# Kernel tuning notes

Measured on AMD Instinct MI355X. Metric: run time of the kernel, lower is better.

## Reference

```python
import jax, jax.numpy as jnp
import numpy as np

B, T, S1, S2 = 8, 64, 128, 128
TD, SD, V, PAD = 512, 512, 32000, 0
EXT = V + S1 + S2
EPS = 1e-5


def _ln(x):
    # F.layer_norm with no affine params (biased variance, eps=1e-5)
    m = x.mean(axis=-1, keepdims=True)
    v = ((x - m) ** 2).mean(axis=-1, keepdims=True)
    return (x - m) / jnp.sqrt(v + EPS)


def _cross_attention(q, k, q_mask, k_mask, attn_w, attn_b, v_vec):
    # attn(cat(q,k)) == q @ Wq^T + k @ Wk^T + b, computed without materializing the concat
    Wq = attn_w[:, :TD]          # [TD, TD] (query part of weight: cat order is (query, key))
    Wk = attn_w[:, TD:]          # [TD, SD]
    sq = jnp.einsum('btd,ed->bte', q, Wq)   # [B,T,TD]
    sk = jnp.einsum('bsd,ed->bse', k, Wk)   # [B,S,TD]
    energy = jnp.tanh(sq[:, :, None, :] + sk[:, None, :, :] + attn_b)  # [B,T,S,TD]
    scores = jnp.einsum('btse,e->bts', energy, v_vec)                  # [B,T,S]
    out_att = scores * k_mask[:, None, :] * q_mask[:, :, None]
    masked = jnp.where((k_mask == PAD)[:, None, :], -jnp.inf, scores)
    attn = jax.nn.softmax(masked, axis=-1)
    weight = jnp.einsum('bts,bsd->btd', attn, k) * q_mask[:, :, None]  # [B,T,SD]
    return out_att, weight


def _scatter_copy(att, map_idx):
    # index_put_(accumulate=True) into [B,T,EXT]
    copy = jnp.zeros((B, T, EXT), dtype=att.dtype)
    b_idx = jnp.arange(B)[:, None, None]
    t_idx = jnp.arange(T)[None, :, None]
    m_idx = map_idx[:, None, :]
    return copy.at[b_idx, t_idx, m_idx].add(att)


def setup_inputs() -> dict:
    key = jax.random.key(0)
    ks = jax.random.split(key, 14)
    sc = 0.02
    return {
        'tgt_dec_out': jax.random.normal(ks[0], (B, T, TD), jnp.float32),
        'src1_key': jax.random.normal(ks[1], (B, S1, SD), jnp.float32),
        'src2_key': jax.random.normal(ks[2], (B, S2, SD), jnp.float32),
        'src1_map_idx': jax.random.randint(ks[3], (B, S1), 0, EXT),
        'src2_map_idx': jax.random.randint(ks[4], (B, S2), 0, EXT),
        'out_fc_w': jax.random.normal(ks[5], (V, TD), jnp.float32) * sc,
        'out_fc_b': jnp.zeros((V,), jnp.float32),
        'attn1_w': jax.random.normal(ks[6], (TD, SD + TD), jnp.float32) * sc,
        'attn1_b': jnp.zeros((TD,), jnp.float32),
        'v1': jax.random.normal(ks[7], (TD,), jnp.float32) * sc,
        'attn2_w': jax.random.normal(ks[8], (TD, SD + TD), jnp.float32) * sc,
        'attn2_b': jnp.zeros((TD,), jnp.float32),
        'v2': jax.random.normal(ks[9], (TD,), jnp.float32) * sc,
        'gate_w': jax.random.normal(ks[10], (3, 2 * SD + TD), jnp.float32) * sc,
        'gate_b': jnp.zeros((3,), jnp.float32),
    }


def reference(tgt_dec_out, src1_key, src2_key, src1_map_idx, src2_map_idx,
              out_fc_w, out_fc_b, attn1_w, attn1_b, v1, attn2_w, attn2_b, v2,
              gate_w, gate_b):
    tgt_output = _ln(jnp.einsum('btd,vd->btv', tgt_dec_out, out_fc_w) + out_fc_b)
    tgt_output = jnp.pad(tgt_output, ((0, 0), (0, 0), (0, S1 + S2)), constant_values=float(PAD))

    tgt_mask = jnp.sign(jnp.abs(tgt_dec_out).sum(-1))   # [B,T]
    src1_mask = jnp.sign(jnp.abs(src1_key).sum(-1))     # [B,S1]
    src2_mask = jnp.sign(jnp.abs(src2_key).sum(-1))     # [B,S2]

    att1, c1 = _cross_attention(tgt_dec_out, src1_key, tgt_mask, src1_mask, attn1_w, attn1_b, v1)
    att1 = _ln(att1)
    copy_output1 = _scatter_copy(att1, src1_map_idx)

    att2, c2 = _cross_attention(tgt_dec_out, src2_key, tgt_mask, src2_mask, attn2_w, attn2_b, v2)
    att2 = _ln(att2)
    copy_output2 = _scatter_copy(att2, src2_map_idx)

    gate_in = jnp.concatenate([tgt_dec_out, c1, c2], axis=-1)  # [B,T,TD+2*SD]
    p = jax.nn.softmax(jnp.einsum('btd,pd->btp', gate_in, gate_w) + gate_b, axis=-1)  # [B,T,3]

    output = (tgt_output * p[..., 0:1]
              + copy_output1 * p[..., 1:2]
              + copy_output2 * p[..., 2:3])
    return output
```

## Files before the change

kernel.cpp:

```cpp
#include <hip/hip_runtime.h>

#define NB 8
#define NT 64
#define NS 128
#define TDIM 512
#define NV 32000
#define NEXT 32256
#define NBT 512
#define LNEPS 1e-5f
#define CLG 2.8853900817779268f

typedef unsigned short u16;
typedef __attribute__((ext_vector_type(8))) short short8;
typedef __attribute__((ext_vector_type(4))) short s16x4;
typedef __attribute__((ext_vector_type(4))) float f32x4;

__device__ __forceinline__ float bf2f(u16 u){ union{unsigned int i; float f;} v; v.i = ((unsigned int)u)<<16; return v.f; }
__device__ __forceinline__ u16 f2bf(float f){ union{float f; unsigned int i;} v; v.f=f; unsigned int r = v.i + 0x7FFFu + ((v.i>>16)&1u); return (u16)(r>>16); }
__device__ __forceinline__ float wsum(float v){
  v += __shfl_xor(v,32); v += __shfl_xor(v,16); v += __shfl_xor(v,8);
  v += __shfl_xor(v,4);  v += __shfl_xor(v,2);  v += __shfl_xor(v,1); return v; }
__device__ __forceinline__ float wmax(float v){
  v = fmaxf(v,__shfl_xor(v,32)); v = fmaxf(v,__shfl_xor(v,16)); v = fmaxf(v,__shfl_xor(v,8));
  v = fmaxf(v,__shfl_xor(v,4));  v = fmaxf(v,__shfl_xor(v,2));  v = fmaxf(v,__shfl_xor(v,1)); return v; }

#define GL2LDS(gp, lp) __builtin_amdgcn_global_load_lds( \
    (__attribute__((address_space(1))) void*)(void*)(gp), \
    (__attribute__((address_space(3))) void*)(void*)(lp), 16, 0, 0)

__global__ __launch_bounds__(256) void k_cast(const float* tgt, const float* s1, const float* s2,
    const float* a1w, const float* a2w,
    u16* tgtb, u16* s1b, u16* s2b, u16* a1wb, u16* a2wb, float* msk)
{
  int blk = blockIdx.x;
  const float* src; u16* dst; int base;
  if(blk < 128){       src=tgt; dst=tgtb;  base=blk; }
  else if(blk < 384){  src=s1;  dst=s1b;   base=blk-128; }
  else if(blk < 640){  src=s2;  dst=s2b;   base=blk-384; }
  else if(blk < 896){  src=a1w; dst=a1wb;  base=blk-640; }
  else {               src=a2w; dst=a2wb;  base=blk-896; }
  size_t off = (size_t)base*2048 + (size_t)threadIdx.x*8;
  float4 x0 = *(const float4*)(src+off);
  float4 x1 = *(const float4*)(src+off+4);
  float xs[8] = {x0.x,x0.y,x0.z,x0.w,x1.x,x1.y,x1.z,x1.w};
  short8 r;
  #pragma unroll
  for(int j=0;j<8;++j) r[j] = (short)f2bf(xs[j]);
  *(short8*)(dst+off) = r;
  if(blk < 640){
    float a = 0.f;
    #pragma unroll
    for(int j=0;j<8;++j) a += fabsf(xs[j]);
    a = wsum(a);
    if((threadIdx.x&63)==0){
      int w = threadIdx.x>>6;
      int midx;
      if(blk<128)      midx = blk*4 + w;
      else if(blk<384) midx = 512 + (blk-128)*4 + w;
      else             midx = 1536 + (blk-384)*4 + w;
      msk[midx] = (a>0.f) ? 1.f : 0.f;
    }
  }
}

template<int MODE>
__device__ __forceinline__ void gemm_core(const u16* A, int lda, const u16* W, int ldw,
    float* Cf, int ldc, const float* bias, int K, int bm, int bn, float scale)
{
  __shared__ u16 Al[128*32];
  __shared__ u16 Wl[128*32];
  const int tid = threadIdx.x, lane = tid&63, wv = tid>>6;
  const int wm = wv>>1, wn = wv&1;
  const int fr = lane&15, fq = lane>>4;
  const int lrow = lane>>2;
  const int lcol = (lane&3)*8;
  f32x4 acc[4][4] = {};
  for(int k0=0;k0<K;k0+=32){
    #pragma unroll
    for(int r=0;r<2;++r){
      int c = wv + 4*r;
      int row = c*16 + lrow;
      const u16* ga = A + (size_t)(bm+row)*lda + k0 + lcol;
      const u16* gw = W + (size_t)(bn+row)*ldw + k0 + lcol;
      GL2LDS(ga, &Al[c*512]);
      GL2LDS(gw, &Wl[c*512]);
    }
    __syncthreads();
    short8 af[4], bfr[4];
    #pragma unroll
    for(int m=0;m<4;++m) af[m] = *(const short8*)&Al[(wm*64 + m*16 + fr)*32 + fq*8];
    #pragma unroll
    for(int n=0;n<4;++n) bfr[n] = *(const short8*)&Wl[(wn*64 + n*16 + fr)*32 + fq*8];
    #pragma unroll
    for(int m=0;m<4;++m)
      #pragma unroll
      for(int n=0;n<4;++n)
        acc[m][n] = __builtin_amdgcn_mfma_f32_16x16x32_bf16(af[m], bfr[n], acc[m][n], 0,0,0);
    __syncthreads();
  }
  #pragma unroll
  for(int m=0;m<4;++m)
    #pragma unroll
    for(int n=0;n<4;++n)
      #pragma unroll
      for(int i=0;i<4;++i){
        int row = bm + wm*64 + m*16 + fq*4 + i;
        int col = bn + wn*64 + n*16 + fr;
        float bv = bias ? bias[col] : 0.f;
        Cf[(size_t)row*ldc + col] = (acc[m][n][i] + bv)*scale;
      }
}

__global__ __launch_bounds__(256) void k_proj(const u16* tgt, const u16* s1, const u16* s2,
    const u16* w1, const u16* w2, const float* b1, const float* b2,
    float* sq1, float* sk1, float* sq2, float* sk2)
{
  int z = blockIdx.z;
  int Mt = (z&1) ? 1024 : 512;
  int bm = blockIdx.y*128; if(bm >= Mt) return;
  const u16* A = (z&1) ? ((z>>1) ? s2 : s1) : tgt;
  const u16* W = ((z>>1) ? w2 : w1) + ((z&1) ? TDIM : 0);
  float* Cf = (z==0) ? sq1 : (z==1) ? sk1 : (z==2) ? sq2 : sk2;
  const float* bias = (z&1) ? nullptr : ((z>>1) ? b2 : b1);
  gemm_core<2>(A, TDIM, W, 2*TDIM, Cf, TDIM, bias, TDIM, bm, blockIdx.x*128, CLG);
}

__global__ __launch_bounds__(256) void k_big(const u16* A, const float* Wf, const float* bias,
                                             u16* logits, float2* pstats)
{
  int lid = (blockIdx.x&7)*125 + (blockIdx.x>>3);
  int bm = (lid&3)*128, bn = (lid>>2)*128;
  __shared__ u16 Al[128*32];
  __shared__ u16 Wl[128*32];
  __shared__ float ps_s[2][128], pq_s[2][128];
  const int tid = threadIdx.x, lane = tid&63, wv = tid>>6;
  const int wm = wv>>1, wn = wv&1;
  const int fr = lane&15, fq = lane>>4;
  const int lrow = lane>>2;
  const int lcol = (lane&3)*8;
  f32x4 acc[4][4] = {};
  for(int k0=0;k0<512;k0+=32){
    #pragma unroll
    for(int r=0;r<2;++r){
      int c = wv + 4*r;
      int row = c*16 + lrow;
      GL2LDS(A + (size_t)(bm+row)*512 + k0 + lcol, &Al[c*512]);
    }
    #pragma unroll
    for(int j=0;j<4;++j){
      int idx = j*256 + tid;
      int row = idx>>3, c = idx&7;
      float4 w4 = *(const float4*)(Wf + (size_t)(bn+row)*512 + k0 + c*4);
      s16x4 o;
      o[0]=(short)f2bf(w4.x); o[1]=(short)f2bf(w4.y); o[2]=(short)f2bf(w4.z); o[3]=(short)f2bf(w4.w);
      *(s16x4*)&Wl[row*32 + c*4] = o;
    }
    __syncthreads();
    short8 af[4], bfr[4];
    #pragma unroll
    for(int m=0;m<4;++m) af[m] = *(const short8*)&Al[(wm*64 + m*16 + fr)*32 + fq*8];
    #pragma unroll
    for(int n=0;n<4;++n) bfr[n] = *(const short8*)&Wl[(wn*64 + n*16 + fr)*32 + fq*8];
    #pragma unroll
    for(int m=0;m<4;++m)
      #pragma unroll
      for(int n=0;n<4;++n)
        acc[m][n] = __builtin_amdgcn_mfma_f32_16x16x32_bf16(af[m], bfr[n], acc[m][n], 0,0,0);
    __syncthreads();
  }
  #pragma unroll
  for(int m=0;m<4;++m){
    float rs_[4]={0,0,0,0}, rq_[4]={0,0,0,0};
    #pragma unroll
    for(int n=0;n<4;++n)
      #pragma unroll
      for(int i=0;i<4;++i){
        int row = bm + wm*64 + m*16 + fq*4 + i;
        int col = bn + wn*64 + n*16 + fr;
        float v = acc[m][n][i] + bias[col];
        logits[(size_t)row*NV + col] = f2bf(v);
        rs_[i] += v; rq_[i] += v*v;
      }
    #pragma unroll
    for(int i=0;i<4;++i){
      float a=rs_[i], q=rq_[i];
      a+=__shfl_xor(a,1); a+=__shfl_xor(a,2); a+=__shfl_xor(a,4); a+=__shfl_xor(a,8);
      q+=__shfl_xor(q,1); q+=__shfl_xor(q,2); q+=__shfl_xor(q,4); q+=__shfl_xor(q,8);
      if(fr==0){ int lr = wm*64 + m*16 + fq*4 + i; ps_s[wn][lr]=a; pq_s[wn][lr]=q; }
    }
  }
  __syncthreads();
  if(tid<128){
    float2 pv;
    pv.x = ps_s[0][tid]+ps_s[1][tid];
    pv.y = pq_s[0][tid]+pq_s[1][tid];
    pstats[(size_t)(bm+tid)*250 + (lid>>2)] = pv;
  }
}

__global__ __launch_bounds__(256) void k_energy(
  const float* sq1, const float* sq2, const float* sk1, const float* sk2,
  const float* v1p, const float* v2p, float* pene)
{
  int lid = (blockIdx.x&7)*128 + (blockIdx.x>>3);
  int src = lid>>9, b = (lid>>6)&7, tc = (lid>>4)&3, sc = (lid>>2)&3, eq = lid&3;
  int tid = threadIdx.x;
  const float* SQ = src? sq2:sq1;
  const float* SK = src? sk2:sk1;
  const float* vp = src? v2p:v1p;
  int t0 = tc*16, s0 = sc*32;
  int strow = tid&31, trow = tid>>5;

  __shared__ float sk_lds[32*65];
  float acc_a = 0.f, acc_b = 0.f;
  const float* sqa = SQ + (size_t)(b*64 + t0 + trow)*512;
  const float* sqb = sqa + 8*512;

  for(int ec=eq*2; ec<eq*2+2; ++ec){
    {
      int r = tid>>3, c0 = (tid&7)*8;
      const float* sp = SK + (size_t)(b*128 + s0 + r)*512 + ec*64 + c0;
      float4 A0 = *(const float4*)sp;
      float4 A1 = *(const float4*)(sp+4);
      float* dp = &sk_lds[r*65 + c0];
      dp[0]=A0.x; dp[1]=A0.y; dp[2]=A0.z; dp[3]=A0.w;
      dp[4]=A1.x; dp[5]=A1.y; dp[6]=A1.z; dp[7]=A1.w;
    }
    __syncthreads();
    #pragma unroll
    for(int sub=0; sub<4; ++sub){
      int e0 = ec*64 + sub*16;
      float4 V0 = *(const float4*)(vp+e0),    V1 = *(const float4*)(vp+e0+4);
      float4 V2 = *(const float4*)(vp+e0+8),  V3 = *(const float4*)(vp+e0+12);
      float4 QA0 = *(const float4*)(sqa+e0),  QA1 = *(const float4*)(sqa+e0+4);
      float4 QA2 = *(const float4*)(sqa+e0+8),QA3 = *(const float4*)(sqa+e0+12);
      float4 QB0 = *(const float4*)(sqb+e0),  QB1 = *(const float4*)(sqb+e0+4);
      float4 QB2 = *(const float4*)(sqb+e0+8),QB3 = *(const float4*)(sqb+e0+12);
      float vv[16] = {V0.x,V0.y,V0.z,V0.w,V1.x,V1.y,V1.z,V1.w,V2.x,V2.y,V2.z,V2.w,V3.x,V3.y,V3.z,V3.w};
      float qa[16] = {QA0.x,QA0.y,QA0.z,QA0.w,QA1.x,QA1.y,QA1.z,QA1.w,QA2.x,QA2.y,QA2.z,QA2.w,QA3.x,QA3.y,QA3.z,QA3.w};
      float qb[16] = {QB0.x,QB0.y,QB0.z,QB0.w,QB1.x,QB1.y,QB1.z,QB1.w,QB2.x,QB2.y,QB2.z,QB2.w,QB3.x,QB3.y,QB3.z,QB3.w};
      const float* skr = &sk_lds[strow*65 + sub*16];
      #pragma unroll
      for(int e=0;e<16;++e){
        float skv = skr[e];
        float ya = qa[e] + skv;
        float yb = qb[e] + skv;
        float ra = __builtin_amdgcn_rcpf(__builtin_amdgcn_exp2f(ya) + 1.f);
        float rb = __builtin_amdgcn_rcpf(__builtin_amdgcn_exp2f(yb) + 1.f);
        acc_a = __builtin_fmaf(vv[e], ra, acc_a);
        acc_b = __builtin_fmaf(vv[e], rb, acc_b);
      }
    }
    __syncthreads();
  }
  size_t ia = (size_t)((eq*2+src)*512 + b*64 + t0 + trow)*128 + s0 + strow;
  pene[ia] = acc_a;
  pene[ia + 8*128] = acc_b;
}

__global__ __launch_bounds__(256) void k_sm(
  const float* pene, const float* v1p, const float* v2p,
  const float* k1g, const float* k2g, const float* msk,
  float* al1, float* al2, float* c1, float* c2)
{
  int lid = (blockIdx.x&7)*32 + (blockIdx.x>>3);
  int src = lid>>7, b = (lid>>4)&7, tq = lid&15;
  int tid = threadIdx.x, lane = tid&63, wv = tid>>6;
  int t = tq*4 + wv, bt = b*64 + t;
  const float* vp = src? v2p:v1p;
  const float* kg = src? k2g:k1g;
  float* al = src? al2:al1;
  float* cc = src? c2:c1;
  const float* km_g = msk + 512 + src*1024 + b*128;
  __shared__ float aw_lds[4][132];
  __shared__ float qm_lds[4];

  {
    float vsp = 0.f;
    #pragma unroll
    for(int r2=0;r2<8;++r2) vsp += vp[lane + 64*r2];
    float Vsum = wsum(vsp);
    float qm = msk[bt];
    float km0 = km_g[lane], km1 = km_g[lane+64];
    size_t pbase = (size_t)(src*512 + bt)*128;
    float p0a = pene[pbase + lane]          + pene[pbase + 131072 + lane];
    float p0b = pene[pbase + 262144 + lane] + pene[pbase + 393216 + lane];
    float p1a = pene[pbase + lane + 64]          + pene[pbase + 131072 + lane + 64];
    float p1b = pene[pbase + 262144 + lane + 64] + pene[pbase + 393216 + lane + 64];
    float s0v = Vsum - 2.f*(p0a + p0b);
    float s1v = Vsum - 2.f*(p1a + p1b);
    float a0 = s0v*km0*qm, a1 = s1v*km1*qm;
    float sm = wsum(a0+a1), sqq = wsum(a0*a0+a1*a1);
    float m0 = km0!=0.f ? s0v : -1e30f;
    float m1 = km1!=0.f ? s1v : -1e30f;
    float mx = wmax(fmaxf(m0,m1));
    float e0 = km0!=0.f ? __expf(s0v-mx) : 0.f;
    float e1 = km1!=0.f ? __expf(s1v-mx) : 0.f;
    float den = wsum(e0+e1);
    float mean = sm/128.f;
    float inv  = rsqrtf(sqq/128.f - mean*mean + LNEPS);
    al[(size_t)bt*128 + lane]      = (a0-mean)*inv;
    al[(size_t)bt*128 + lane + 64] = (a1-mean)*inv;
    float rden = 1.f/den;
    aw_lds[wv][lane]      = e0*rden;
    aw_lds[wv][lane+64]   = e1*rden;
    if(lane==0) qm_lds[wv] = qm;
  }
  __syncthreads();
  {
    float acc[4][2] = {};
    const float* kb = kg + (size_t)b*128*512;
    for(int s=0;s<128;++s){
      float kv0 = kb[(size_t)s*512 + tid];
      float kv1 = kb[(size_t)s*512 + tid + 256];
      #pragma unroll
      for(int w=0;w<4;++w){
        float a = aw_lds[w][s];
        acc[w][0] = __builtin_fmaf(a, kv0, acc[w][0]);
        acc[w][1] = __builtin_fmaf(a, kv1, acc[w][1]);
      }
    }
    #pragma unroll
    for(int w=0;w<4;++w){
      float qm = qm_lds[w];
      size_t o = (size_t)(b*64 + tq*4 + w)*512;
      cc[o + tid]       = qm*acc[w][0];
      cc[o + tid + 256] = qm*acc[w][1];
    }
  }
}

__global__ __launch_bounds__(256) void k_out(const u16* logits, const float2* pstats,
    const float* al1, const float* al2, const float* c1, const float* c2,
    const float* tgt, const float* gw, const float* gb,
    const int* map1, const int* map2, float* out)
{
  int row = blockIdx.x>>2, q = blockIdx.x&3, b = row>>6;
  int tid = threadIdx.x, lane = tid&63, wv = tid>>6;
  __shared__ float gred[4][3], rs[4], rq[4], st[2], pl_s[3];
  __shared__ int hkey[1024];
  __shared__ float hval[1024];
  __shared__ unsigned int bmap[252];

  #pragma unroll
  for(int r=0;r<4;++r){ hkey[tid+256*r] = -1; hval[tid+256*r] = 0.f; }
  if(tid < 252) bmap[tid] = 0u;

  {
    float t0v = tgt[(size_t)row*512+tid], t1v = tgt[(size_t)row*512+tid+256];
    float c10 = c1[(size_t)row*512+tid],  c11 = c1[(size_t)row*512+tid+256];
    float c20 = c2[(size_t)row*512+tid],  c21 = c2[(size_t)row*512+tid+256];
    #pragma unroll
    for(int p=0;p<3;++p){
      const float* gp = gw + p*1536;
      float a = gp[tid]*t0v + gp[tid+256]*t1v
              + gp[512+tid]*c10 + gp[768+tid]*c11
              + gp[1024+tid]*c20 + gp[1280+tid]*c21;
      a = wsum(a);
      if(lane==0) gred[wv][p] = a;
    }
  }
  {
    float s=0.f, qv=0.f;
    if(tid < 250){ float2 pv = pstats[(size_t)row*250 + tid]; s = pv.x; qv = pv.y; }
    s = wsum(s); qv = wsum(qv);
    if(lane==0){ rs[wv]=s; rq[wv]=qv; }
  }
  __syncthreads();
  if(tid==0){
    float S = rs[0]+rs[1]+rs[2]+rs[3];
    float Q = rq[0]+rq[1]+rq[2]+rq[3];
    float mean = S/(float)NV;
    float var  = Q/(float)NV - mean*mean;
    st[0] = mean; st[1] = rsqrtf(var+LNEPS);
    float g0 = gred[0][0]+gred[1][0]+gred[2][0]+gred[3][0] + gb[0];
    float g1 = gred[0][1]+gred[1][1]+gred[2][1]+gred[3][1] + gb[1];
    float g2 = gred[0][2]+gred[1][2]+gred[2][2]+gred[3][2] + gb[2];
    float m = fmaxf(g0, fmaxf(g1, g2));
    float e0=__expf(g0-m), e1=__expf(g1-m), e2=__expf(g2-m);
    float sI = 1.f/(e0+e1+e2);
    pl_s[0]=e0*sI; pl_s[1]=e1*sI; pl_s[2]=e2*sI;
  }
  __syncthreads();

  int elo = q*8064;
  {
    int src = tid>>7, sl = tid&127;
    int e = (src ? map2 : map1)[b*128 + sl];
    if(e >= elo && e < elo+8064){
      float val = pl_s[1+src] * (src ? al2 : al1)[(size_t)row*128 + sl];
      unsigned int h = ((unsigned int)e * 2654435761u) >> 22;
      for(;;){
        int old = atomicCAS(&hkey[h], -1, e);
        if(old == -1 || old == e){ atomicAdd(&hval[h], val); break; }
        h = (h+1) & 1023;
      }
      int rel = e - elo;
      atomicOr(&bmap[rel>>5], 1u << (rel&31));
    }
  }
  __syncthreads();

  float mean = st[0], inv = st[1], p0 = pl_s[0];
  const u16* Lr = logits + (size_t)row*NV;
  float* orow = out + (size_t)row*NEXT;
  for(int i=q*2016+tid; i<(q+1)*2016; i+=256){
    int e0 = i*4;
    float4 r;
    if(e0 < NV){
      const u16* L = &Lr[e0];
      r.x = p0*(bf2f(L[0])-mean)*inv;
      r.y = p0*(bf2f(L[1])-mean)*inv;
      r.z = p0*(bf2f(L[2])-mean)*inv;
      r.w = p0*(bf2f(L[3])-mean)*inv;
    } else { r.x=r.y=r.z=r.w=0.f; }
    int rel = e0 - elo;
    unsigned int w4 = (bmap[rel>>5] >> (rel&31)) & 0xFu;
    if(w4){
      #pragma unroll
      for(int j=0;j<4;++j){
        if(w4 & (1u<<j)){
          int e = e0 + j;
          unsigned int h = ((unsigned int)e * 2654435761u) >> 22;
          while(hkey[h] != e) h = (h+1) & 1023;
          float pv = hval[h];
          if(j==0) r.x += pv; else if(j==1) r.y += pv; else if(j==2) r.z += pv; else r.w += pv;
        }
      }
    }
    *(float4*)&orow[e0] = r;
  }
}

extern "C" void kernel_launch(void* const* d_in, const int* in_sizes, int n_in,
                              void* d_out, int out_size, void* d_ws, size_t ws_size,
                              hipStream_t stream)
{
  const float* tgt  = (const float*)d_in[0];
  const float* s1k  = (const float*)d_in[1];
  const float* s2k  = (const float*)d_in[2];
  const int*   map1 = (const int*)d_in[3];
  const int*   map2 = (const int*)d_in[4];
  const float* ofw  = (const float*)d_in[5];
  const float* ofb  = (const float*)d_in[6];
  const float* a1w  = (const float*)d_in[7];
  const float* a1b  = (const float*)d_in[8];
  const float* v1   = (const float*)d_in[9];
  const float* a2w  = (const float*)d_in[10];
  const float* a2b  = (const float*)d_in[11];
  const float* v2   = (const float*)d_in[12];
  const float* gw   = (const float*)d_in[13];
  const float* gb   = (const float*)d_in[14];

  float* wsf   = (float*)d_ws;
  float* sq1   = wsf;
  float* sq2   = wsf + 262144;
  float* sk1   = wsf + 524288;
  float* sk2   = wsf + 1048576;
  float* al1   = wsf + 1572864;
  float* al2   = wsf + 1638400;
  float* msk   = wsf + 1705984;
  float* c1    = wsf + 1709568;
  float* c2    = wsf + 1971712;
  float* pene  = wsf + 2233856;
  float2* pstats = (float2*)(wsf + 2758144);
  u16*  logits = (u16*)(wsf + 3014144);
  u16*  tgtb   = (u16*)(wsf + 11206144);
  u16*  s1b    = (u16*)(wsf + 11337216);
  u16*  s2b    = (u16*)(wsf + 11599360);
  u16*  a1wb   = (u16*)(wsf + 11861504);
  u16*  a2wb   = (u16*)(wsf + 12123648);
  float* out   = (float*)d_out;

  k_cast   <<<1152, 256, 0, stream>>>(tgt, s1k, s2k, a1w, a2w, tgtb, s1b, s2b, a1wb, a2wb, msk);
  k_proj   <<<dim3(4,8,4), 256, 0, stream>>>(tgtb, s1b, s2b, a1wb, a2wb, a1b, a2b, sq1, sk1, sq2, sk2);
  k_energy <<<1024, 256, 0, stream>>>(sq1, sq2, sk1, sk2, v1, v2, pene);
  k_sm     <<<256, 256, 0, stream>>>(pene, v1, v2, s1k, s2k, msk, al1, al2, c1, c2);
  k_big    <<<1000, 256, 0, stream>>>(tgtb, ofw, ofb, logits, pstats);
  k_out    <<<2048, 256, 0, stream>>>(logits, pstats, al1, al2, c1, c2, tgt, gw, gb, map1, map2, out);
}
```

Measured before the change: 122.4 us.

## Pre-cast output weight to bf16, merge projection and logits GEMMs, stage logits stores

The fp32 output weight is now cast to bf16 in the cast kernel instead of inside the logits GEMM's inner loop, so that GEMM can load both operands with direct global-to-LDS loads. The projection GEMM and the large logits GEMM become one launch, with extra blocks handling the projections. Logits are staged through LDS and written as 16-byte row-contiguous stores instead of scattered 2-byte stores. The cost is an extra pass that reads the 64MB fp32 weight and writes a 32MB bf16 copy every call, plus more LDS and more syncs per block.

```diff
diff --git a/kernel.cpp b/kernel.cpp
--- a/kernel.cpp
+++ b/kernel.cpp
@@ -12,7 +12,6 @@
 
 typedef unsigned short u16;
 typedef __attribute__((ext_vector_type(8))) short short8;
-typedef __attribute__((ext_vector_type(4))) short s16x4;
 typedef __attribute__((ext_vector_type(4))) float f32x4;
 
 __device__ __forceinline__ float bf2f(u16 u){ union{unsigned int i; float f;} v; v.i = ((unsigned int)u)<<16; return v.f; }
@@ -29,8 +28,8 @@
     (__attribute__((address_space(3))) void*)(void*)(lp), 16, 0, 0)
 
 __global__ __launch_bounds__(256) void k_cast(const float* tgt, const float* s1, const float* s2,
-    const float* a1w, const float* a2w,
-    u16* tgtb, u16* s1b, u16* s2b, u16* a1wb, u16* a2wb, float* msk)
+    const float* a1w, const float* a2w, const float* ofw,
+    u16* tgtb, u16* s1b, u16* s2b, u16* a1wb, u16* a2wb, u16* ofwb, float* msk)
 {
   int blk = blockIdx.x;
   const float* src; u16* dst; int base;
@@ -38,7 +37,8 @@
   else if(blk < 384){  src=s1;  dst=s1b;   base=blk-128; }
   else if(blk < 640){  src=s2;  dst=s2b;   base=blk-384; }
   else if(blk < 896){  src=a1w; dst=a1wb;  base=blk-640; }
-  else {               src=a2w; dst=a2wb;  base=blk-896; }
+  else if(blk < 1152){ src=a2w; dst=a2wb;  base=blk-896; }
+  else {               src=ofw; dst=ofwb;  base=blk-1152; }
   size_t off = (size_t)base*2048 + (size_t)threadIdx.x*8;
   float4 x0 = *(const float4*)(src+off);
   float4 x1 = *(const float4*)(src+off+4);
@@ -63,12 +63,9 @@
   }
 }
 
-template<int MODE>
-__device__ __forceinline__ void gemm_core(const u16* A, int lda, const u16* W, int ldw,
+__device__ __forceinline__ void gemm_core2(u16* Al, u16* Wl, const u16* A, int lda, const u16* W, int ldw,
     float* Cf, int ldc, const float* bias, int K, int bm, int bn, float scale)
 {
-  __shared__ u16 Al[128*32];
-  __shared__ u16 Wl[128*32];
   const int tid = threadIdx.x, lane = tid&63, wv = tid>>6;
   const int wm = wv>>1, wn = wv&1;
   const int fr = lane&15, fq = lane>>4;
@@ -111,28 +108,32 @@
       }
 }
 
-__global__ __launch_bounds__(256) void k_proj(const u16* tgt, const u16* s1, const u16* s2,
-    const u16* w1, const u16* w2, const float* b1, const float* b2,
+__global__ __launch_bounds__(256) void k_bigproj(const u16* A, const u16* W, const float* bias,
+    u16* logits, float2* pstats,
+    const u16* s1, const u16* s2, const u16* w1, const u16* w2,
+    const float* b1, const float* b2,
     float* sq1, float* sk1, float* sq2, float* sk2)
 {
-  int z = blockIdx.z;
-  int Mt = (z&1) ? 1024 : 512;
-  int bm = blockIdx.y*128; if(bm >= Mt) return;
-  const u16* A = (z&1) ? ((z>>1) ? s2 : s1) : tgt;
-  const u16* W = ((z>>1) ? w2 : w1) + ((z&1) ? TDIM : 0);
-  float* Cf = (z==0) ? sq1 : (z==1) ? sk1 : (z==2) ? sq2 : sk2;
-  const float* bias = (z&1) ? nullptr : ((z>>1) ? b2 : b1);
-  gemm_core<2>(A, TDIM, W, 2*TDIM, Cf, TDIM, bias, TDIM, bm, blockIdx.x*128, CLG);
-}
-
-__global__ __launch_bounds__(256) void k_big(const u16* A, const float* Wf, const float* bias,
-                                             u16* logits, float2* pstats)
-{
-  int lid = (blockIdx.x&7)*125 + (blockIdx.x>>3);
-  int bm = (lid&3)*128, bn = (lid>>2)*128;
   __shared__ u16 Al[128*32];
   __shared__ u16 Wl[128*32];
   __shared__ float ps_s[2][128], pq_s[2][128];
+  __shared__ u16 c16[2][16][136];
+
+  if(blockIdx.x >= 1000){
+    int p = blockIdx.x - 1000;
+    int z = p>>5, y = (p>>2)&7, x = p&3;
+    int Mt = (z&1) ? 1024 : 512;
+    int bm = y*128; if(bm >= Mt) return;
+    const u16* Ap = (z&1) ? ((z>>1) ? s2 : s1) : A;
+    const u16* Wp = ((z>>1) ? w2 : w1) + ((z&1) ? TDIM : 0);
+    float* Cf = (z==0) ? sq1 : (z==1) ? sk1 : (z==2) ? sq2 : sk2;
+    const float* bp = (z&1) ? nullptr : ((z>>1) ? b2 : b1);
+    gemm_core2(Al, Wl, Ap, TDIM, Wp, 2*TDIM, Cf, TDIM, bp, TDIM, bm, x*128, CLG);
+    return;
+  }
+
+  int lid = (blockIdx.x&7)*125 + (blockIdx.x>>3);
+  int bm = (lid&3)*128, bn = (lid>>2)*128;
   const int tid = threadIdx.x, lane = tid&63, wv = tid>>6;
   const int wm = wv>>1, wn = wv&1;
   const int fr = lane&15, fq = lane>>4;
@@ -145,15 +146,7 @@
       int c = wv + 4*r;
       int row = c*16 + lrow;
       GL2LDS(A + (size_t)(bm+row)*512 + k0 + lcol, &Al[c*512]);
-    }
-    #pragma unroll
-    for(int j=0;j<4;++j){
-      int idx = j*256 + tid;
-      int row = idx>>3, c = idx&7;
-      float4 w4 = *(const float4*)(Wf + (size_t)(bn+row)*512 + k0 + c*4);
-      s16x4 o;
-      o[0]=(short)f2bf(w4.x); o[1]=(short)f2bf(w4.y); o[2]=(short)f2bf(w4.z); o[3]=(short)f2bf(w4.w);
-      *(s16x4*)&Wl[row*32 + c*4] = o;
+      GL2LDS(W + (size_t)(bn+row)*512 + k0 + lcol, &Wl[c*512]);
     }
     __syncthreads();
     short8 af[4], bfr[4];
@@ -168,6 +161,7 @@
         acc[m][n] = __builtin_amdgcn_mfma_f32_16x16x32_bf16(af[m], bfr[n], acc[m][n], 0,0,0);
     __syncthreads();
   }
+
   #pragma unroll
   for(int m=0;m<4;++m){
     float rs_[4]={0,0,0,0}, rq_[4]={0,0,0,0};
@@ -175,10 +169,9 @@
     for(int n=0;n<4;++n)
       #pragma unroll
       for(int i=0;i<4;++i){
-        int row = bm + wm*64 + m*16 + fq*4 + i;
         int col = bn + wn*64 + n*16 + fr;
         float v = acc[m][n][i] + bias[col];
-        logits[(size_t)row*NV + col] = f2bf(v);
+        c16[wm][fq*4+i][wn*64 + n*16 + fr] = f2bf(v);
         rs_[i] += v; rq_[i] += v*v;
       }
     #pragma unroll
@@ -188,8 +181,17 @@
       q+=__shfl_xor(q,1); q+=__shfl_xor(q,2); q+=__shfl_xor(q,4); q+=__shfl_xor(q,8);
       if(fr==0){ int lr = wm*64 + m*16 + fq*4 + i; ps_s[wn][lr]=a; pq_s[wn][lr]=q; }
     }
-  }
-  __syncthreads();
+    __syncthreads();
+    {
+      int band = tid>>7, r = (tid>>3)&15, c0 = (tid&7)*16;
+      int grow = bm + band*64 + m*16 + r;
+      short8 o0 = *(const short8*)&c16[band][r][c0];
+      short8 o1 = *(const short8*)&c16[band][r][c0+8];
+      *(short8*)&logits[(size_t)grow*NV + bn + c0]     = o0;
+      *(short8*)&logits[(size_t)grow*NV + bn + c0 + 8] = o1;
+    }
+    __syncthreads();
+  }
   if(tid<128){
     float2 pv;
     pv.x = ps_s[0][tid]+ps_s[1][tid];
@@ -470,12 +472,13 @@
   u16*  s2b    = (u16*)(wsf + 11599360);
   u16*  a1wb   = (u16*)(wsf + 11861504);
   u16*  a2wb   = (u16*)(wsf + 12123648);
+  u16*  ofwb   = (u16*)(wsf + 12385792);
   float* out   = (float*)d_out;
 
-  k_cast   <<<1152, 256, 0, stream>>>(tgt, s1k, s2k, a1w, a2w, tgtb, s1b, s2b, a1wb, a2wb, msk);
-  k_proj   <<<dim3(4,8,4), 256, 0, stream>>>(tgtb, s1b, s2b, a1wb, a2wb, a1b, a2b, sq1, sk1, sq2, sk2);
+  k_cast   <<<9152, 256, 0, stream>>>(tgt, s1k, s2k, a1w, a2w, ofw, tgtb, s1b, s2b, a1wb, a2wb, ofwb, msk);
+  k_bigproj<<<1128, 256, 0, stream>>>(tgtb, ofwb, ofb, logits, pstats,
+                                      s1b, s2b, a1wb, a2wb, a1b, a2b, sq1, sk1, sq2, sk2);
   k_energy <<<1024, 256, 0, stream>>>(sq1, sq2, sk1, sk2, v1, v2, pene);
   k_sm     <<<256, 256, 0, stream>>>(pene, v1, v2, s1k, s2k, msk, al1, al2, c1, c2);
-  k_big    <<<1000, 256, 0, stream>>>(tgtb, ofw, ofb, logits, pstats);
   k_out    <<<2048, 256, 0, stream>>>(logits, pstats, al1, al2, c1, c2, tgt, gw, gb, map1, map2, out);
 }
```

Result: faster. 119.4 us (-2.5%).
